# Optimization experiments

Hardware: AMD Instinct MI355X
Metric: run time of the kernel (lower is better)

Reference implementation:

```python
import jax, jax.numpy as jnp
import numpy as np

EPS = 1e-12  # torch F.normalize default eps


def setup_inputs() -> dict:
    key = jax.random.key(0)
    k1, k2, k3 = jax.random.split(key, 3)
    ns, d_in, n_feat, n_classes = 16384, 512, 256, 1000
    x = jax.random.normal(k1, (ns, d_in), dtype=jnp.float32)
    W = jax.random.normal(k2, (d_in, n_feat), dtype=jnp.float32) * 0.05
    # class prototypes: L2-normalized embeddings, one per seen class (seen_c == n_classes)
    means = jax.random.normal(k3, (n_classes, n_feat), dtype=jnp.float32)
    means = means / jnp.maximum(jnp.linalg.norm(means, axis=1, keepdims=True), EPS)
    return {"x": x, "W": W, "means": means, "t": 0}


def reference(x, W, means, t):
    # forward_training: backbone + L2 normalization along feature dim
    feats = x @ W                                   # [ns, n_feat]
    preds = feats / jnp.maximum(jnp.linalg.norm(feats, axis=1, keepdims=True), EPS)
    # deployment forward: nearest prototype by negative dot product
    # original: per-sample dist = -means @ pred^T; dist.min(0) -> class index
    dist = -(preds @ means.T)                       # [ns, seen_c]
    classpred = jnp.argmin(dist, axis=1)            # first min on ties, matches torch
    n_classes = means.shape[0]
    out = jax.nn.one_hot(classpred, n_classes, dtype=jnp.float32)  # [ns, n_classes]
    return out
```

## Files before the change

kernel.cpp:

```cpp
#include <hip/hip_runtime.h>
#include <float.h>

#define NS   16384
#define K1   512
#define F    256
#define NC   1000
#define SPB  64
#define NTHR 512
#define NBLK (NS / SPB)


typedef _Float16 half8  __attribute__((ext_vector_type(8)));
typedef float    float4v __attribute__((ext_vector_type(4)));

#define M_OFF 262144

__global__ void prep(const float* __restrict__ W, const float* __restrict__ means,
                     _Float16* __restrict__ ws) {
    int g = blockIdx.x * blockDim.x + threadIdx.x;
    if (g < 16384) {
        int lane = g & 63, tile = g >> 6;
        int ks = tile >> 4, nt = tile & 15;
        int k0 = ks * 32 + (lane >> 4) * 8;
        int n  = nt * 16 + (lane & 15);
        half8 hv, lv;
#pragma unroll
        for (int j = 0; j < 8; ++j) {
            float v = W[(size_t)(k0 + j) * F + n] * 16.0f;
            _Float16 hi = (_Float16)v;
            hv[j] = hi;
            lv[j] = (_Float16)(v - (float)hi);
        }
        _Float16* d = ws + (size_t)tile * 1024 + (size_t)lane * 8;
        *reinterpret_cast<half8*>(d)       = hv;
        *reinterpret_cast<half8*>(d + 512) = lv;
    } else {
        int gm = g - 16384;
        int lane = gm & 63, tile = gm >> 6;
        int ks = tile >> 6, gt = tile & 63;
        int k0 = ks * 32 + (lane >> 4) * 8;
        int c  = gt * 16 + (lane & 15);
        half8 hv, lv;
#pragma unroll
        for (int j = 0; j < 8; ++j) {
            float v = (c < NC) ? means[(size_t)c * F + k0 + j] * 16.0f : 0.0f;
            _Float16 hi = (_Float16)v;
            hv[j] = hi;
            lv[j] = (_Float16)(v - (float)hi);
        }
        _Float16* d = ws + M_OFF + (size_t)tile * 1024 + (size_t)lane * 8;
        *reinterpret_cast<half8*>(d)       = hv;
        *reinterpret_cast<half8*>(d + 512) = lv;
    }
}

#define MFMA(a, b, c) __builtin_amdgcn_mfma_f32_16x16x32_f16((a), (b), (c), 0, 0, 0)

__attribute__((amdgpu_flat_work_group_size(NTHR, NTHR), amdgpu_waves_per_eu(2, 4)))
__global__ void fused_mfma(const float* __restrict__ x,
                           const _Float16* __restrict__ ws,
                           float* __restrict__ out) {
    __shared__ _Float16 xsh[2][64][40];
    __shared__ _Float16 xsl[2][64][40];
    __shared__ _Float16 fh[64][264];
    __shared__ _Float16 fl[64][264];
    __shared__ float cand_v[64][8];
    __shared__ int   cand_i[64][8];
    __shared__ int   bidx[64];

    const int tid  = threadIdx.x;
    const int lane = tid & 63;
    const int w    = tid >> 6;
    const int quad = lane >> 4;
    const int cl   = lane & 15;
    const int s0   = blockIdx.x * SPB;

    const int xrow = tid >> 3;
    const int xc4  = (tid & 7) * 4;

    float4v acc1[2][4];
#pragma unroll
    for (int p = 0; p < 2; ++p)
#pragma unroll
        for (int mt = 0; mt < 4; ++mt)
            acc1[p][mt] = (float4v){0.f, 0.f, 0.f, 0.f};

    const _Float16* wsrc = ws + ((size_t)(w * 2) << 10) + ((size_t)lane << 3);
    half8 wbh[2][2], wbl[2][2];
#pragma unroll
    for (int p = 0; p < 2; ++p) {
        wbh[0][p] = *reinterpret_cast<const half8*>(wsrc + p * 1024);
        wbl[0][p] = *reinterpret_cast<const half8*>(wsrc + p * 1024 + 512);
    }

    float4v xv = __builtin_nontemporal_load(
        reinterpret_cast<const float4v*>(x + (size_t)(s0 + xrow) * K1 + xc4));

#pragma unroll
    for (int ks = 0; ks < 16; ++ks) {
        const int buf = ks & 1;
        {
#pragma unroll
            for (int j = 0; j < 4; ++j) {
                float v = xv[j] * 8.0f;
                _Float16 hi = (_Float16)v;
                xsh[buf][xrow][xc4 + j] = hi;
                xsl[buf][xrow][xc4 + j] = (_Float16)(v - (float)hi);
            }
        }
        if (ks < 15)
            xv = __builtin_nontemporal_load(
                reinterpret_cast<const float4v*>(
                    x + (size_t)(s0 + xrow) * K1 + (ks + 1) * 32 + xc4));
        __syncthreads();
        if (ks < 15) {
#pragma unroll
            for (int p = 0; p < 2; ++p) {
                wbh[buf ^ 1][p] = *reinterpret_cast<const half8*>(
                    wsrc + (size_t)(ks + 1) * 16384 + p * 1024);
                wbl[buf ^ 1][p] = *reinterpret_cast<const half8*>(
                    wsrc + (size_t)(ks + 1) * 16384 + p * 1024 + 512);
            }
        }
        half8 ah[4], al[4];
#pragma unroll
        for (int mt = 0; mt < 4; ++mt) {
            ah[mt] = *reinterpret_cast<const half8*>(&xsh[buf][mt * 16 + cl][quad * 8]);
            al[mt] = *reinterpret_cast<const half8*>(&xsl[buf][mt * 16 + cl][quad * 8]);
        }
#pragma unroll
        for (int p = 0; p < 2; ++p)
#pragma unroll
            for (int mt = 0; mt < 4; ++mt) {
                acc1[p][mt] = MFMA(ah[mt], wbh[buf][p], acc1[p][mt]);
                acc1[p][mt] = MFMA(ah[mt], wbl[buf][p], acc1[p][mt]);
                acc1[p][mt] = MFMA(al[mt], wbh[buf][p], acc1[p][mt]);
            }
    }

#pragma unroll
    for (int p = 0; p < 2; ++p)
#pragma unroll
        for (int mt = 0; mt < 4; ++mt)
#pragma unroll
            for (int r = 0; r < 4; ++r) {
                int srow = mt * 16 + quad * 4 + r;
                int n    = (w * 2 + p) * 16 + cl;
                float v  = acc1[p][mt][r];
                _Float16 hi = (_Float16)v;
                fh[srow][n] = hi;
                fl[srow][n] = (_Float16)(v - (float)hi);
            }
    __syncthreads();

    float4v acc2[4][8];
#pragma unroll
    for (int mt = 0; mt < 4; ++mt)
#pragma unroll
        for (int gt = 0; gt < 8; ++gt)
            acc2[mt][gt] = (float4v){0.f, 0.f, 0.f, 0.f};

    const _Float16* mbase = ws + M_OFF + ((size_t)(w * 8) << 10) + ((size_t)lane << 3);

    half8 mh[2], ml[2];
    mh[0] = *reinterpret_cast<const half8*>(mbase);
    ml[0] = *reinterpret_cast<const half8*>(mbase + 512);

    const float4v z4 = (float4v){0.f, 0.f, 0.f, 0.f};
    const int NF4 = NC / 4;

#pragma unroll
    for (int ks = 0; ks < 8; ++ks) {
        half8 fah[4], fal[4];
#pragma unroll
        for (int mt = 0; mt < 4; ++mt) {
            fah[mt] = *reinterpret_cast<const half8*>(
                &fh[mt * 16 + cl][ks * 32 + quad * 8]);
            fal[mt] = *reinterpret_cast<const half8*>(
                &fl[mt * 16 + cl][ks * 32 + quad * 8]);
        }
#pragma unroll
        for (int j = 0; j < 4; ++j) {
            int q = (ks * 4 + j) * NTHR + tid;
            if (q < SPB * NF4) {
                int row = q / NF4;
                int c4  = q - row * NF4;
                __builtin_nontemporal_store(
                    z4, reinterpret_cast<float4v*>(
                            out + (size_t)(s0 + row) * NC + c4 * 4));
            }
        }
#pragma unroll
        for (int gt = 0; gt < 8; ++gt) {
            const int ii = ks * 8 + gt;
            const int cb = ii & 1;
            if (ii < 63) {
                const _Float16* src = mbase +
                    (size_t)(((ii + 1) >> 3) * 65536 + ((ii + 1) & 7) * 1024);
                mh[cb ^ 1] = *reinterpret_cast<const half8*>(src);
                ml[cb ^ 1] = *reinterpret_cast<const half8*>(src + 512);
            }
#pragma unroll
            for (int mt = 0; mt < 4; ++mt) {
                acc2[mt][gt] = MFMA(fah[mt], mh[cb], acc2[mt][gt]);
                acc2[mt][gt] = MFMA(fah[mt], ml[cb], acc2[mt][gt]);
                acc2[mt][gt] = MFMA(fal[mt], mh[cb], acc2[mt][gt]);
            }
        }
    }

#pragma unroll
    for (int mt = 0; mt < 4; ++mt)
#pragma unroll
        for (int r = 0; r < 4; ++r) {
            float v  = -FLT_MAX;
            int   ix = 0x7FFFFFFF;
#pragma unroll
            for (int nt = 0; nt < 8; ++nt) {
                int c = (w * 8 + nt) * 16 + cl;
                if (c < NC) {
                    float sc = acc2[mt][nt][r];
                    if (sc > v) { v = sc; ix = c; }
                }
            }
#pragma unroll
            for (int off = 1; off < 16; off <<= 1) {
                float ov = __shfl_xor(v, off, 64);
                int   oi = __shfl_xor(ix, off, 64);
                if (ov > v || (ov == v && oi < ix)) { v = ov; ix = oi; }
            }
            if (cl == 0) {
                int srow = mt * 16 + quad * 4 + r;
                cand_v[srow][w] = v;
                cand_i[srow][w] = ix;
            }
        }
    __syncthreads();

    if (tid < SPB) {
        float v  = cand_v[tid][0];
        int   ix = cand_i[tid][0];
#pragma unroll
        for (int q = 1; q < 8; ++q) {
            float ov = cand_v[tid][q];
            int   oi = cand_i[tid][q];
            if (ov > v || (ov == v && oi < ix)) { v = ov; ix = oi; }
        }
        bidx[tid] = ix;
    }
    __syncthreads();

    if (tid < SPB)
        out[(size_t)(s0 + tid) * NC + bidx[tid]] = 1.0f;
}

extern "C" void kernel_launch(void* const* d_in, const int* in_sizes, int n_in,
                              void* d_out, int out_size, void* d_ws, size_t ws_size,
                              hipStream_t stream) {
    const float* x     = (const float*)d_in[0];
    const float* W     = (const float*)d_in[1];
    const float* means = (const float*)d_in[2];
    float* out         = (float*)d_out;
    _Float16* ws       = (_Float16*)d_ws;

    prep<<<192, 256, 0, stream>>>(W, means, ws);
    fused_mfma<<<NBLK, NTHR, 0, stream>>>(x, ws, out);
}
```

Measured before the change: 132.1 us.

## Move output zero-fill into prep kernel and vectorize x LDS stores

Zeroing of the 16384x1000 one-hot output moves out of the fused MFMA kernel and into extra blocks of the prep launch. The aim is to take the large streaming store work out of the compute kernel's inner loop, so the compute kernel only writes its ones. The x-tile split into fp16 hi/lo is now written to shared memory as 4-wide vectors, and the barrier sits before the next global load of x. The cost is that the zero-fill now runs serially before the main kernel instead of overlapping with MFMA work.

```diff
diff --git a/kernel.cpp b/kernel.cpp
--- a/kernel.cpp
+++ b/kernel.cpp
@@ -11,13 +11,31 @@
 
 
 typedef _Float16 half8  __attribute__((ext_vector_type(8)));
+typedef _Float16 half4v __attribute__((ext_vector_type(4)));
 typedef float    float4v __attribute__((ext_vector_type(4)));
 
 #define M_OFF 262144
 
+#define PREP_BLKS 192
+#define ZERO_BLKS 2048
+
 __global__ void prep(const float* __restrict__ W, const float* __restrict__ means,
-                     _Float16* __restrict__ ws) {
-    int g = blockIdx.x * blockDim.x + threadIdx.x;
+                     _Float16* __restrict__ ws, float* __restrict__ out) {
+    const int bid = blockIdx.x;
+    if (bid >= PREP_BLKS) {
+        const size_t total4 = (size_t)NS * NC / 4;
+        const float4v z4 = (float4v){0.f, 0.f, 0.f, 0.f};
+        size_t base = (size_t)(bid - PREP_BLKS) * 2048 + threadIdx.x;
+#pragma unroll
+        for (int j = 0; j < 8; ++j) {
+            size_t q = base + (size_t)j * 256;
+            if (q < total4)
+                __builtin_nontemporal_store(
+                    z4, reinterpret_cast<float4v*>(out) + q);
+        }
+        return;
+    }
+    int g = bid * blockDim.x + threadIdx.x;
     if (g < 16384) {
         int lane = g & 63, tile = g >> 6;
         int ks = tile >> 4, nt = tile & 15;
@@ -100,19 +118,22 @@
     for (int ks = 0; ks < 16; ++ks) {
         const int buf = ks & 1;
         {
+            half4v hx, lx;
 #pragma unroll
             for (int j = 0; j < 4; ++j) {
                 float v = xv[j] * 8.0f;
                 _Float16 hi = (_Float16)v;
-                xsh[buf][xrow][xc4 + j] = hi;
-                xsl[buf][xrow][xc4 + j] = (_Float16)(v - (float)hi);
-            }
-        }
+                hx[j] = hi;
+                lx[j] = (_Float16)(v - (float)hi);
+            }
+            *reinterpret_cast<half4v*>(&xsh[buf][xrow][xc4]) = hx;
+            *reinterpret_cast<half4v*>(&xsl[buf][xrow][xc4]) = lx;
+        }
+        __syncthreads();
         if (ks < 15)
             xv = __builtin_nontemporal_load(
                 reinterpret_cast<const float4v*>(
                     x + (size_t)(s0 + xrow) * K1 + (ks + 1) * 32 + xc4));
-        __syncthreads();
         if (ks < 15) {
 #pragma unroll
             for (int p = 0; p < 2; ++p) {
@@ -166,9 +187,6 @@
     mh[0] = *reinterpret_cast<const half8*>(mbase);
     ml[0] = *reinterpret_cast<const half8*>(mbase + 512);
 
-    const float4v z4 = (float4v){0.f, 0.f, 0.f, 0.f};
-    const int NF4 = NC / 4;
-
 #pragma unroll
     for (int ks = 0; ks < 8; ++ks) {
         half8 fah[4], fal[4];
@@ -178,17 +196,6 @@
                 &fh[mt * 16 + cl][ks * 32 + quad * 8]);
             fal[mt] = *reinterpret_cast<const half8*>(
                 &fl[mt * 16 + cl][ks * 32 + quad * 8]);
-        }
-#pragma unroll
-        for (int j = 0; j < 4; ++j) {
-            int q = (ks * 4 + j) * NTHR + tid;
-            if (q < SPB * NF4) {
-                int row = q / NF4;
-                int c4  = q - row * NF4;
-                __builtin_nontemporal_store(
-                    z4, reinterpret_cast<float4v*>(
-                            out + (size_t)(s0 + row) * NC + c4 * 4));
-            }
         }
 #pragma unroll
         for (int gt = 0; gt < 8; ++gt) {
@@ -263,6 +270,6 @@
     float* out         = (float*)d_out;
     _Float16* ws       = (_Float16*)d_ws;
 
-    prep<<<192, 256, 0, stream>>>(W, means, ws);
+    prep<<<PREP_BLKS + ZERO_BLKS, 256, 0, stream>>>(W, means, ws, out);
     fused_mfma<<<NBLK, NTHR, 0, stream>>>(x, ws, out);
 }
```

After: 141.3 us. 7.0% more time.
